# Kernel tuning notes

Measured on AMD Instinct MI355X. Metric: run time of the kernel, lower is better.

## Reference

```python
import jax, jax.numpy as jnp
import numpy as np

NUM_PHONEMES = 512
D = 128  # embed_dim == hidden_channels == out_channels (forced by residuals)
N = 50000
E = 500000
PAD_ID = 0
LN_EPS = 1e-5


def setup_inputs() -> dict:
    key = jax.random.key(0)
    ks = jax.random.split(key, 12)
    node_ids = jax.random.randint(ks[0], (N,), 0, NUM_PHONEMES)
    edge_index = jax.random.randint(ks[1], (2, E), 0, N)
    emb = jax.random.normal(ks[2], (NUM_PHONEMES, D), jnp.float32) * 0.05
    emb = emb.at[PAD_ID].set(0.0)  # padding_idx row zeroed
    W1 = jax.random.normal(ks[3], (D, D), jnp.float32) * (1.0 / np.sqrt(D))
    b1 = jnp.zeros((D,), jnp.float32)
    W2 = jax.random.normal(ks[4], (D, D), jnp.float32) * (1.0 / np.sqrt(D))
    b2 = jnp.zeros((D,), jnp.float32)
    g1 = jnp.ones((D,), jnp.float32)
    beta1 = jnp.zeros((D,), jnp.float32)
    g2 = jnp.ones((D,), jnp.float32)
    beta2 = jnp.zeros((D,), jnp.float32)
    return {"node_ids": node_ids, "edge_index": edge_index, "emb": emb,
            "W1": W1, "b1": b1, "W2": W2, "b2": b2,
            "g1": g1, "beta1": beta1, "g2": g2, "beta2": beta2}


def _gcn_conv(x, src, dst, W, b):
    """PyG GCNConv with add_self_loops=True, normalize=True.
    out = D^{-1/2} (A + I) D^{-1/2} (x W) + b, deg computed after self-loops."""
    n = x.shape[0]
    loop = jnp.arange(n, dtype=src.dtype)
    src_f = jnp.concatenate([src, loop])  # [E+N]
    dst_f = jnp.concatenate([dst, loop])
    deg = jax.ops.segment_sum(jnp.ones_like(dst_f, dtype=x.dtype), dst_f,
                              num_segments=n)  # >=1 due to self-loops
    dis = jax.lax.rsqrt(deg)
    norm = dis[src_f] * dis[dst_f]  # [E+N]
    h = x @ W  # [N, D_out]
    msg = h[src_f] * norm[:, None]  # [E+N, D_out] gather (memory-bound)
    out = jax.ops.segment_sum(msg, dst_f, num_segments=n)  # scatter-add
    return out + b


def _layernorm(x, g, b):
    mu = jnp.mean(x, axis=-1, keepdims=True)
    var = jnp.mean(jnp.square(x - mu), axis=-1, keepdims=True)
    return (x - mu) * jax.lax.rsqrt(var + LN_EPS) * g + b


def reference(node_ids, edge_index, emb, W1, b1, W2, b2, g1, beta1, g2, beta2):
    src, dst = edge_index[0], edge_index[1]
    x = emb[node_ids]  # embedding lookup [N, D]
    h1 = _gcn_conv(x, src, dst, W1, b1)
    x = _layernorm(x + h1, g1, beta1)  # dropout is identity in eval mode
    h2 = _gcn_conv(x, src, dst, W2, b2)
    x = _layernorm(x + h2, g2, beta2)
    return x
```

## Files before the change

### kernel.cpp

```cpp
#include <hip/hip_runtime.h>

#define DD 128
#define CAP 32
#define SPILL_MAX 4096

typedef __attribute__((ext_vector_type(8))) short short8;
typedef __attribute__((ext_vector_type(4))) float float4v;

static __device__ __forceinline__ unsigned short f2bf(float x) {
    unsigned u = __builtin_bit_cast(unsigned, x);
    u += 0x7fffu + ((u >> 16) & 1u);
    return (unsigned short)(u >> 16);
}
static __device__ __forceinline__ float bflo(unsigned u) {
    return __builtin_bit_cast(float, u << 16);
}
static __device__ __forceinline__ float bfhi(unsigned u) {
    return __builtin_bit_cast(float, u & 0xffff0000u);
}

__global__ __launch_bounds__(256) void k_init(const float* __restrict__ emb,
                                              const float* __restrict__ W1,
                                              const float* __restrict__ W2,
                                              unsigned* __restrict__ embW1b,
                                              unsigned short* __restrict__ Wb,
                                              const int* __restrict__ src,
                                              const int* __restrict__ dst,
                                              const int* __restrict__ node_ids,
                                              int* __restrict__ cursor,
                                              unsigned* __restrict__ recs,
                                              int* __restrict__ spillCnt,
                                              int* __restrict__ spill_d,
                                              int* __restrict__ spill_r, int E) {
    int blk = blockIdx.x;
    if (blk < 128) {
        int w = threadIdx.x >> 6;
        int t = threadIdx.x & 63;
        int p = blk * 4 + w;
        int c0 = t * 2, c1 = t * 2 + 1;
        float s0 = 0.f, s1 = 0.f;
#pragma unroll 8
        for (int k = 0; k < DD; k++) {
            float e = emb[p * DD + k];
            s0 += e * W1[k * DD + c0];
            s1 += e * W1[k * DD + c1];
        }
        embW1b[p * 64 + t] = (unsigned)f2bf(s0) | ((unsigned)f2bf(s1) << 16);
    } else if (blk < 136) {
        int t = (blk - 128) * 256 + threadIdx.x;
        int nt = t >> 8, ks = (t >> 6) & 3, lane = t & 63;
        int n = nt * 16 + (lane & 15);
        int kbase = ks * 32 + (lane >> 4) * 8;
        unsigned short* o = Wb + (size_t)t * 8;
#pragma unroll
        for (int j = 0; j < 8; j++)
            o[j] = f2bf(W2[(kbase + j) * DD + n]);
    } else {
        int base = ((blk - 136) * 256 + threadIdx.x) * 4;
        if (base >= E) return;
#pragma unroll
        for (int u = 0; u < 4; u++) {
            int e = base + u;
            if (e >= E) break;
            int s = src[e], d = dst[e];
            unsigned rec = (unsigned)s | ((unsigned)node_ids[s] << 16);
            int pos = atomicAdd(&cursor[d], 1);
            if (pos < CAP) {
                recs[(size_t)d * CAP + pos] = rec;
            } else {
                int sp = atomicAdd(spillCnt, 1);
                if (sp < SPILL_MAX) { spill_d[sp] = d; spill_r[sp] = (int)rec; }
            }
        }
    }
}

__global__ __launch_bounds__(256, 4) void k_node1(const int* __restrict__ cursor,
                                               const unsigned* __restrict__ recs,
                                               const int* __restrict__ node_ids,
                                               const float* __restrict__ emb,
                                               const unsigned* __restrict__ embW1b,
                                               const int* __restrict__ spillCnt,
                                               const int* __restrict__ spill_d,
                                               const int* __restrict__ spill_r,
                                               const float* __restrict__ b1,
                                               const float* __restrict__ g1,
                                               const float* __restrict__ beta1,
                                               unsigned* __restrict__ x1b,
                                               float* __restrict__ disf, int N) {
    int gid = blockIdx.x * blockDim.x + threadIdx.x;
    int wave = gid >> 6;
    int lane = threadIdx.x & 63;
    int qtr = lane >> 4;
    int l = lane & 15;
    int qbase = lane & 48;
    int i = wave * 4 + qtr;
    if (i >= N) return;
    int dg = cursor[i];
    int dgc = (dg < CAP) ? dg : CAP;
    unsigned rv0 = recs[(size_t)i * CAP + l];
    unsigned rv1 = recs[(size_t)i * CAP + 16 + l];
    int c = l * 8;
    float a0 = 0.f, a1 = 0.f, a2 = 0.f, a3 = 0.f, a4 = 0.f, a5 = 0.f, a6 = 0.f, a7 = 0.f;
    for (int j0 = 0; j0 < dgc; j0 += 8) {
        unsigned rvs = (j0 < 16) ? rv0 : rv1;
        const uint4* ap[8]; const int* cp[8]; float nn[8];
#pragma unroll
        for (int q = 0; q < 8; q++) {
            int e = j0 + q;
            int ec = (e < dgc) ? e : (dgc - 1);
            unsigned rec = __shfl(rvs, qbase + (ec & 15), 64);
            nn[q] = (e < dgc) ? 1.f : 0.f;
            ap[q] = (const uint4*)(embW1b + ((rec >> 16) & 511u) * 64 + l * 4);
            cp[q] = cursor + (rec & 0xFFFFu);
        }
        uint4 buf[8]; int cb[8];
#pragma unroll
        for (int q = 0; q < 8; q++) { buf[q] = *ap[q]; cb[q] = *cp[q]; }
#pragma unroll
        for (int q = 0; q < 8; q++) {
            float n = rsqrtf((float)cb[q] + 1.f) * nn[q];
            uint4 a = buf[q];
            a0 += bflo(a.x) * n; a1 += bfhi(a.x) * n;
            a2 += bflo(a.y) * n; a3 += bfhi(a.y) * n;
            a4 += bflo(a.z) * n; a5 += bfhi(a.z) * n;
            a6 += bflo(a.w) * n; a7 += bfhi(a.w) * n;
        }
    }
    if (dg > CAP) {
        int sc = *spillCnt; if (sc > SPILL_MAX) sc = SPILL_MAX;
        for (int j = 0; j < sc; j++) {
            if (spill_d[j] == i) {
                unsigned rec = (unsigned)spill_r[j];
                int s = rec & 0xFFFFu;
                float n = rsqrtf((float)cursor[s] + 1.0f);
                uint4 a = *(const uint4*)(embW1b + ((rec >> 16) & 511u) * 64 + l * 4);
                a0 += bflo(a.x) * n; a1 += bfhi(a.x) * n;
                a2 += bflo(a.y) * n; a3 += bfhi(a.y) * n;
                a4 += bflo(a.z) * n; a5 += bfhi(a.z) * n;
                a6 += bflo(a.w) * n; a7 += bfhi(a.w) * n;
            }
        }
    }
    float di = rsqrtf((float)dg + 1.0f);
    int pid = node_ids[i];
    float4 ev0 = *(const float4*)(emb + (size_t)pid * DD + c);
    float4 ev1 = *(const float4*)(emb + (size_t)pid * DD + c + 4);
    uint4 hw = *(const uint4*)(embW1b + pid * 64 + l * 4);
    float4 bb0 = *(const float4*)(b1 + c);
    float4 bb1 = *(const float4*)(b1 + c + 4);
    float v0 = ev0.x + di * (a0 + di * bflo(hw.x)) + bb0.x;
    float v1 = ev0.y + di * (a1 + di * bfhi(hw.x)) + bb0.y;
    float v2 = ev0.z + di * (a2 + di * bflo(hw.y)) + bb0.z;
    float v3 = ev0.w + di * (a3 + di * bfhi(hw.y)) + bb0.w;
    float v4 = ev1.x + di * (a4 + di * bflo(hw.z)) + bb1.x;
    float v5 = ev1.y + di * (a5 + di * bfhi(hw.z)) + bb1.y;
    float v6 = ev1.z + di * (a6 + di * bflo(hw.w)) + bb1.z;
    float v7 = ev1.w + di * (a7 + di * bfhi(hw.w)) + bb1.w;
    float sum = v0 + v1 + v2 + v3 + v4 + v5 + v6 + v7;
#pragma unroll
    for (int o = 8; o >= 1; o >>= 1) sum += __shfl_xor(sum, o, 64);
    float mu = sum * (1.f / DD);
    float d0 = v0 - mu, d1 = v1 - mu, d2 = v2 - mu, d3 = v3 - mu;
    float d4 = v4 - mu, d5 = v5 - mu, d6 = v6 - mu, d7 = v7 - mu;
    float ss = d0 * d0 + d1 * d1 + d2 * d2 + d3 * d3 + d4 * d4 + d5 * d5 + d6 * d6 + d7 * d7;
#pragma unroll
    for (int o = 8; o >= 1; o >>= 1) ss += __shfl_xor(ss, o, 64);
    float r = rsqrtf(ss * (1.f / DD) + 1e-5f);
    float4 gg0 = *(const float4*)(g1 + c);
    float4 gg1 = *(const float4*)(g1 + c + 4);
    float4 be0 = *(const float4*)(beta1 + c);
    float4 be1 = *(const float4*)(beta1 + c + 4);
    float o0 = d0 * r * gg0.x + be0.x;
    float o1 = d1 * r * gg0.y + be0.y;
    float o2 = d2 * r * gg0.z + be0.z;
    float o3 = d3 * r * gg0.w + be0.w;
    float o4 = d4 * r * gg1.x + be1.x;
    float o5 = d5 * r * gg1.y + be1.y;
    float o6 = d6 * r * gg1.z + be1.z;
    float o7 = d7 * r * gg1.w + be1.w;
    uint4 pk;
    pk.x = (unsigned)f2bf(o0) | ((unsigned)f2bf(o1) << 16);
    pk.y = (unsigned)f2bf(o2) | ((unsigned)f2bf(o3) << 16);
    pk.z = (unsigned)f2bf(o4) | ((unsigned)f2bf(o5) << 16);
    pk.w = (unsigned)f2bf(o6) | ((unsigned)f2bf(o7) << 16);
    *(uint4*)(x1b + (size_t)i * 64 + l * 4) = pk;
    if (l == 0) disf[i] = di;
}

__global__ __launch_bounds__(256, 4) void k_node2(const int* __restrict__ cursor,
                                               const unsigned* __restrict__ recs,
                                               const unsigned* __restrict__ x1b,
                                               const float* __restrict__ disf,
                                               const int* __restrict__ spillCnt,
                                               const int* __restrict__ spill_d,
                                               const int* __restrict__ spill_r,
                                               const float* __restrict__ b2,
                                               const float* __restrict__ g2,
                                               const float* __restrict__ beta2,
                                               const unsigned short* __restrict__ Wb,
                                               float* __restrict__ out, int N) {
    __shared__ unsigned tileA[4][16 * 68];
    int wv = threadIdx.x >> 6;
    int lane = threadIdx.x & 63;
    int qtr = lane >> 4;
    int l = lane & 15;
    int qbase = lane & 48;
    int wbase = (blockIdx.x * 4 + wv) * 16;
    unsigned* myT = &tileA[wv][0];
#pragma unroll 1
    for (int k = 0; k < 4; k++) {
        int rr = k * 4 + qtr;
        int i = wbase + rr;
        uint4 pk = make_uint4(0, 0, 0, 0);
        if (i < N) {
            int dg = cursor[i];
            int dgc = (dg < CAP) ? dg : CAP;
            unsigned rv0 = recs[(size_t)i * CAP + l];
            unsigned rv1 = recs[(size_t)i * CAP + 16 + l];
            float a0 = 0.f, a1 = 0.f, a2 = 0.f, a3 = 0.f, a4 = 0.f, a5 = 0.f, a6 = 0.f, a7 = 0.f;
            for (int j0 = 0; j0 < dgc; j0 += 8) {
                unsigned rvs = (j0 < 16) ? rv0 : rv1;
                const uint4* ap[8]; const float* fp[8]; float nn[8];
#pragma unroll
                for (int q = 0; q < 8; q++) {
                    int e = j0 + q;
                    int ec = (e < dgc) ? e : (dgc - 1);
                    unsigned rec = __shfl(rvs, qbase + (ec & 15), 64);
                    unsigned s = rec & 0xFFFFu;
                    nn[q] = (e < dgc) ? 1.f : 0.f;
                    ap[q] = (const uint4*)(x1b + (size_t)s * 64 + l * 4);
                    fp[q] = disf + s;
                }
                uint4 buf[8]; float fb[8];
#pragma unroll
                for (int q = 0; q < 8; q++) { buf[q] = *ap[q]; fb[q] = *fp[q]; }
#pragma unroll
                for (int q = 0; q < 8; q++) {
                    float n = fb[q] * nn[q];
                    uint4 a = buf[q];
                    a0 += bflo(a.x) * n; a1 += bfhi(a.x) * n;
                    a2 += bflo(a.y) * n; a3 += bfhi(a.y) * n;
                    a4 += bflo(a.z) * n; a5 += bfhi(a.z) * n;
                    a6 += bflo(a.w) * n; a7 += bfhi(a.w) * n;
                }
            }
            if (dg > CAP) {
                int sc = *spillCnt; if (sc > SPILL_MAX) sc = SPILL_MAX;
                for (int j = 0; j < sc; j++) {
                    if (spill_d[j] == i) {
                        unsigned s = (unsigned)spill_r[j] & 0xFFFFu;
                        float n = disf[s];
                        uint4 a = *(const uint4*)(x1b + (size_t)s * 64 + l * 4);
                        a0 += bflo(a.x) * n; a1 += bfhi(a.x) * n;
                        a2 += bflo(a.y) * n; a3 += bfhi(a.y) * n;
                        a4 += bflo(a.z) * n; a5 += bfhi(a.z) * n;
                        a6 += bflo(a.w) * n; a7 += bfhi(a.w) * n;
                    }
                }
            }
            float di = disf[i];
            uint4 xv = *(const uint4*)(x1b + (size_t)i * 64 + l * 4);
            float z0 = a0 + di * bflo(xv.x);
            float z1 = a1 + di * bfhi(xv.x);
            float z2 = a2 + di * bflo(xv.y);
            float z3 = a3 + di * bfhi(xv.y);
            float z4 = a4 + di * bflo(xv.z);
            float z5 = a5 + di * bfhi(xv.z);
            float z6 = a6 + di * bflo(xv.w);
            float z7 = a7 + di * bfhi(xv.w);
            pk.x = (unsigned)f2bf(z0) | ((unsigned)f2bf(z1) << 16);
            pk.y = (unsigned)f2bf(z2) | ((unsigned)f2bf(z3) << 16);
            pk.z = (unsigned)f2bf(z4) | ((unsigned)f2bf(z5) << 16);
            pk.w = (unsigned)f2bf(z6) | ((unsigned)f2bf(z7) << 16);
        }
        *(uint4*)(myT + rr * 68 + l * 4) = pk;
    }
    __syncthreads();
    short8 afr[4];
    const char* tb = (const char*)myT;
#pragma unroll
    for (int ks = 0; ks < 4; ks++)
        afr[ks] = *(const short8*)(tb + l * 272 + ks * 64 + qtr * 16);
    const short8* bp = (const short8*)Wb;
    float4v acc[8];
#pragma unroll
    for (int nt = 0; nt < 8; nt++) {
        float4v a = {0.f, 0.f, 0.f, 0.f};
#pragma unroll
        for (int ks = 0; ks < 4; ks++)
            a = __builtin_amdgcn_mfma_f32_16x16x32_bf16(afr[ks], bp[(nt * 4 + ks) * 64 + lane], a, 0, 0, 0);
        acc[nt] = a;
    }
    float dvarr[4];
    {
        float4 dv4 = *(const float4*)(disf + wbase + qtr * 4);
        dvarr[0] = dv4.x; dvarr[1] = dv4.y; dvarr[2] = dv4.z; dvarr[3] = dv4.w;
    }
#pragma unroll
    for (int r = 0; r < 4; r++) {
        int rowg = wbase + qtr * 4 + r;
        if (rowg < N) {
            float di = dvarr[r];
            float vv[8]; float sum = 0.f;
#pragma unroll
            for (int nt = 0; nt < 8; nt++) {
                unsigned xw = x1b[(size_t)rowg * 64 + nt * 8 + (l >> 1)];
                float xr = (l & 1) ? bfhi(xw) : bflo(xw);
                vv[nt] = xr + di * acc[nt][r] + b2[nt * 16 + l];
                sum += vv[nt];
            }
#pragma unroll
            for (int o = 8; o >= 1; o >>= 1) sum += __shfl_xor(sum, o, 64);
            float mu = sum * (1.f / DD);
            float ss = 0.f;
#pragma unroll
            for (int nt = 0; nt < 8; nt++) { float d = vv[nt] - mu; vv[nt] = d; ss += d * d; }
#pragma unroll
            for (int o = 8; o >= 1; o >>= 1) ss += __shfl_xor(ss, o, 64);
            float rstd = rsqrtf(ss * (1.f / DD) + 1e-5f);
#pragma unroll
            for (int nt = 0; nt < 8; nt++)
                out[(size_t)rowg * DD + nt * 16 + l] = vv[nt] * rstd * g2[nt * 16 + l] + beta2[nt * 16 + l];
        }
    }
}

extern "C" void kernel_launch(void* const* d_in, const int* in_sizes, int n_in,
                              void* d_out, int out_size, void* d_ws, size_t ws_size,
                              hipStream_t stream) {
    const int* node_ids = (const int*)d_in[0];
    const int* edge_index = (const int*)d_in[1];
    const float* emb   = (const float*)d_in[2];
    const float* W1    = (const float*)d_in[3];
    const float* b1    = (const float*)d_in[4];
    const float* W2    = (const float*)d_in[5];
    const float* b2    = (const float*)d_in[6];
    const float* g1    = (const float*)d_in[7];
    const float* beta1 = (const float*)d_in[8];
    const float* g2    = (const float*)d_in[9];
    const float* beta2 = (const float*)d_in[10];
    const int N = in_sizes[0];
    const int E = in_sizes[1] / 2;
    const int* srcp = edge_index;
    const int* dstp = edge_index + E;
    float* out = (float*)d_out;

    char* base = (char*)d_ws;
    size_t off = 0;
    auto carve = [&](size_t bytes) -> void* {
        void* p = base + off;
        off += (bytes + 255) & ~(size_t)255;
        return p;
    };
    int*      meta   = (int*)carve((size_t)(N + 17) * 4);
    int*      cursor = meta;
    int*      spillCnt = meta + N + 16;
    int*      spill_d = (int*)carve((size_t)SPILL_MAX * 4);
    int*      spill_r = (int*)carve((size_t)SPILL_MAX * 4);
    unsigned* recs   = (unsigned*)carve((size_t)N * CAP * 4);
    unsigned* embW1b = (unsigned*)carve((size_t)512 * 64 * 4);
    unsigned* x1b    = (unsigned*)carve((size_t)(N + 64) * 64 * 4);
    float*    disf   = (float*)carve((size_t)(N + 64) * 4);
    unsigned short* Wb = (unsigned short*)carve((size_t)DD * DD * 2);
    (void)ws_size; (void)n_in; (void)out_size;

    const int TB = 256;
    const int Hb = (E + 1023) / 1024;

    hipMemsetAsync(meta, 0, (size_t)(N + 17) * 4, stream);
    k_init<<<136 + Hb, TB, 0, stream>>>(emb, W1, W2, embW1b, Wb,
                                        srcp, dstp, node_ids, cursor, recs,
                                        spillCnt, spill_d, spill_r, E);

    long long tn = (long long)((N + 3) / 4) * 64;
    int nodeBlocks = (int)((tn + TB - 1) / TB);
    k_node1<<<nodeBlocks, TB, 0, stream>>>(cursor, recs, node_ids, emb, embW1b,
                                           spillCnt, spill_d, spill_r,
                                           b1, g1, beta1, x1b, disf, N);
    int blocks64 = (N + 63) / 64;
    k_node2<<<blocks64, TB, 0, stream>>>(cursor, recs, x1b, disf,
                                         spillCnt, spill_d, spill_r,
                                         b2, g2, beta2, Wb, out, N);
}
```

Baseline: 167.3 us.

## Restructure k_node2 to 16 rows per block with split-N MFMA and LDS epilogue

k_node2 now handles 16 rows per 256-thread block instead of 64, with each wave aggregating one neighbour row per quarter-wave in a single pass rather than looping over four rows. The 16x128 MFMA output is split across the four waves (two column tiles each) and staged through a shared fp32 tile, so the LayerNorm epilogue reads contiguous 8-column chunks and writes vectorised float4 outputs. The aim is more blocks and more gather parallelism for latency hiding, plus coalesced output stores. The cost is an extra block barrier and LDS round trip, and four times as many blocks launched.

```diff
diff --git a/kernel.cpp b/kernel.cpp
--- a/kernel.cpp
+++ b/kernel.cpp
@@ -200,130 +200,148 @@
                                                const float* __restrict__ beta2,
                                                const unsigned short* __restrict__ Wb,
                                                float* __restrict__ out, int N) {
-    __shared__ unsigned tileA[4][16 * 68];
+    __shared__ unsigned tileA[16 * 68];
+    __shared__ float tileH[16 * 132];
     int wv = threadIdx.x >> 6;
     int lane = threadIdx.x & 63;
     int qtr = lane >> 4;
     int l = lane & 15;
     int qbase = lane & 48;
-    int wbase = (blockIdx.x * 4 + wv) * 16;
-    unsigned* myT = &tileA[wv][0];
-#pragma unroll 1
-    for (int k = 0; k < 4; k++) {
-        int rr = k * 4 + qtr;
-        int i = wbase + rr;
-        uint4 pk = make_uint4(0, 0, 0, 0);
-        if (i < N) {
-            int dg = cursor[i];
-            int dgc = (dg < CAP) ? dg : CAP;
-            unsigned rv0 = recs[(size_t)i * CAP + l];
-            unsigned rv1 = recs[(size_t)i * CAP + 16 + l];
-            float a0 = 0.f, a1 = 0.f, a2 = 0.f, a3 = 0.f, a4 = 0.f, a5 = 0.f, a6 = 0.f, a7 = 0.f;
-            for (int j0 = 0; j0 < dgc; j0 += 8) {
-                unsigned rvs = (j0 < 16) ? rv0 : rv1;
-                const uint4* ap[8]; const float* fp[8]; float nn[8];
-#pragma unroll
-                for (int q = 0; q < 8; q++) {
-                    int e = j0 + q;
-                    int ec = (e < dgc) ? e : (dgc - 1);
-                    unsigned rec = __shfl(rvs, qbase + (ec & 15), 64);
-                    unsigned s = rec & 0xFFFFu;
-                    nn[q] = (e < dgc) ? 1.f : 0.f;
-                    ap[q] = (const uint4*)(x1b + (size_t)s * 64 + l * 4);
-                    fp[q] = disf + s;
-                }
-                uint4 buf[8]; float fb[8];
-#pragma unroll
-                for (int q = 0; q < 8; q++) { buf[q] = *ap[q]; fb[q] = *fp[q]; }
-#pragma unroll
-                for (int q = 0; q < 8; q++) {
-                    float n = fb[q] * nn[q];
-                    uint4 a = buf[q];
+    int base16 = blockIdx.x * 16;
+    int rr = wv * 4 + qtr;
+    int i = base16 + rr;
+    int c = l * 8;
+    uint4 xv = make_uint4(0, 0, 0, 0);
+    float di = 0.f;
+    uint4 pk = make_uint4(0, 0, 0, 0);
+    if (i < N) {
+        int dg = cursor[i];
+        int dgc = (dg < CAP) ? dg : CAP;
+        unsigned rv0 = recs[(size_t)i * CAP + l];
+        unsigned rv1 = recs[(size_t)i * CAP + 16 + l];
+        float a0 = 0.f, a1 = 0.f, a2 = 0.f, a3 = 0.f, a4 = 0.f, a5 = 0.f, a6 = 0.f, a7 = 0.f;
+        for (int j0 = 0; j0 < dgc; j0 += 8) {
+            unsigned rvs = (j0 < 16) ? rv0 : rv1;
+            const uint4* ap[8]; const float* fp[8]; float nn[8];
+#pragma unroll
+            for (int q = 0; q < 8; q++) {
+                int e = j0 + q;
+                int ec = (e < dgc) ? e : (dgc - 1);
+                unsigned rec = __shfl(rvs, qbase + (ec & 15), 64);
+                unsigned s = rec & 0xFFFFu;
+                nn[q] = (e < dgc) ? 1.f : 0.f;
+                ap[q] = (const uint4*)(x1b + (size_t)s * 64 + l * 4);
+                fp[q] = disf + s;
+            }
+            uint4 buf[8]; float fb[8];
+#pragma unroll
+            for (int q = 0; q < 8; q++) { buf[q] = *ap[q]; fb[q] = *fp[q]; }
+#pragma unroll
+            for (int q = 0; q < 8; q++) {
+                float n = fb[q] * nn[q];
+                uint4 a = buf[q];
+                a0 += bflo(a.x) * n; a1 += bfhi(a.x) * n;
+                a2 += bflo(a.y) * n; a3 += bfhi(a.y) * n;
+                a4 += bflo(a.z) * n; a5 += bfhi(a.z) * n;
+                a6 += bflo(a.w) * n; a7 += bfhi(a.w) * n;
+            }
+        }
+        if (dg > CAP) {
+            int sc = *spillCnt; if (sc > SPILL_MAX) sc = SPILL_MAX;
+            for (int j = 0; j < sc; j++) {
+                if (spill_d[j] == i) {
+                    unsigned s = (unsigned)spill_r[j] & 0xFFFFu;
+                    float n = disf[s];
+                    uint4 a = *(const uint4*)(x1b + (size_t)s * 64 + l * 4);
                     a0 += bflo(a.x) * n; a1 += bfhi(a.x) * n;
                     a2 += bflo(a.y) * n; a3 += bfhi(a.y) * n;
                     a4 += bflo(a.z) * n; a5 += bfhi(a.z) * n;
                     a6 += bflo(a.w) * n; a7 += bfhi(a.w) * n;
                 }
             }
-            if (dg > CAP) {
-                int sc = *spillCnt; if (sc > SPILL_MAX) sc = SPILL_MAX;
-                for (int j = 0; j < sc; j++) {
-                    if (spill_d[j] == i) {
-                        unsigned s = (unsigned)spill_r[j] & 0xFFFFu;
-                        float n = disf[s];
-                        uint4 a = *(const uint4*)(x1b + (size_t)s * 64 + l * 4);
-                        a0 += bflo(a.x) * n; a1 += bfhi(a.x) * n;
-                        a2 += bflo(a.y) * n; a3 += bfhi(a.y) * n;
-                        a4 += bflo(a.z) * n; a5 += bfhi(a.z) * n;
-                        a6 += bflo(a.w) * n; a7 += bfhi(a.w) * n;
-                    }
-                }
-            }
-            float di = disf[i];
-            uint4 xv = *(const uint4*)(x1b + (size_t)i * 64 + l * 4);
-            float z0 = a0 + di * bflo(xv.x);
-            float z1 = a1 + di * bfhi(xv.x);
-            float z2 = a2 + di * bflo(xv.y);
-            float z3 = a3 + di * bfhi(xv.y);
-            float z4 = a4 + di * bflo(xv.z);
-            float z5 = a5 + di * bfhi(xv.z);
-            float z6 = a6 + di * bflo(xv.w);
-            float z7 = a7 + di * bfhi(xv.w);
-            pk.x = (unsigned)f2bf(z0) | ((unsigned)f2bf(z1) << 16);
-            pk.y = (unsigned)f2bf(z2) | ((unsigned)f2bf(z3) << 16);
-            pk.z = (unsigned)f2bf(z4) | ((unsigned)f2bf(z5) << 16);
-            pk.w = (unsigned)f2bf(z6) | ((unsigned)f2bf(z7) << 16);
-        }
-        *(uint4*)(myT + rr * 68 + l * 4) = pk;
+        }
+        di = disf[i];
+        xv = *(const uint4*)(x1b + (size_t)i * 64 + l * 4);
+        float z0 = a0 + di * bflo(xv.x);
+        float z1 = a1 + di * bfhi(xv.x);
+        float z2 = a2 + di * bflo(xv.y);
+        float z3 = a3 + di * bfhi(xv.y);
+        float z4 = a4 + di * bflo(xv.z);
+        float z5 = a5 + di * bfhi(xv.z);
+        float z6 = a6 + di * bflo(xv.w);
+        float z7 = a7 + di * bfhi(xv.w);
+        pk.x = (unsigned)f2bf(z0) | ((unsigned)f2bf(z1) << 16);
+        pk.y = (unsigned)f2bf(z2) | ((unsigned)f2bf(z3) << 16);
+        pk.z = (unsigned)f2bf(z4) | ((unsigned)f2bf(z5) << 16);
+        pk.w = (unsigned)f2bf(z6) | ((unsigned)f2bf(z7) << 16);
+    }
+    *(uint4*)(tileA + rr * 68 + l * 4) = pk;
+    __syncthreads();
+    {
+        short8 afr[4];
+        const char* tb = (const char*)tileA;
+#pragma unroll
+        for (int ks = 0; ks < 4; ks++)
+            afr[ks] = *(const short8*)(tb + l * 272 + ks * 64 + qtr * 16);
+        float dr[4];
+#pragma unroll
+        for (int r = 0; r < 4; r++) {
+            int rw = base16 + qtr * 4 + r;
+            dr[r] = (rw < N) ? disf[rw] : 0.f;
+        }
+        const short8* bp = (const short8*)Wb;
+#pragma unroll
+        for (int t = 0; t < 2; t++) {
+            int nt = wv * 2 + t;
+            float4v acc = {0.f, 0.f, 0.f, 0.f};
+#pragma unroll
+            for (int ks = 0; ks < 4; ks++)
+                acc = __builtin_amdgcn_mfma_f32_16x16x32_bf16(afr[ks], bp[(nt * 4 + ks) * 64 + lane], acc, 0, 0, 0);
+            int col = nt * 16 + l;
+#pragma unroll
+            for (int r = 0; r < 4; r++)
+                tileH[(qtr * 4 + r) * 132 + col] = acc[r] * dr[r];
+        }
     }
     __syncthreads();
-    short8 afr[4];
-    const char* tb = (const char*)myT;
-#pragma unroll
-    for (int ks = 0; ks < 4; ks++)
-        afr[ks] = *(const short8*)(tb + l * 272 + ks * 64 + qtr * 16);
-    const short8* bp = (const short8*)Wb;
-    float4v acc[8];
-#pragma unroll
-    for (int nt = 0; nt < 8; nt++) {
-        float4v a = {0.f, 0.f, 0.f, 0.f};
-#pragma unroll
-        for (int ks = 0; ks < 4; ks++)
-            a = __builtin_amdgcn_mfma_f32_16x16x32_bf16(afr[ks], bp[(nt * 4 + ks) * 64 + lane], a, 0, 0, 0);
-        acc[nt] = a;
-    }
-    float dvarr[4];
-    {
-        float4 dv4 = *(const float4*)(disf + wbase + qtr * 4);
-        dvarr[0] = dv4.x; dvarr[1] = dv4.y; dvarr[2] = dv4.z; dvarr[3] = dv4.w;
-    }
-#pragma unroll
-    for (int r = 0; r < 4; r++) {
-        int rowg = wbase + qtr * 4 + r;
-        if (rowg < N) {
-            float di = dvarr[r];
-            float vv[8]; float sum = 0.f;
-#pragma unroll
-            for (int nt = 0; nt < 8; nt++) {
-                unsigned xw = x1b[(size_t)rowg * 64 + nt * 8 + (l >> 1)];
-                float xr = (l & 1) ? bfhi(xw) : bflo(xw);
-                vv[nt] = xr + di * acc[nt][r] + b2[nt * 16 + l];
-                sum += vv[nt];
-            }
-#pragma unroll
-            for (int o = 8; o >= 1; o >>= 1) sum += __shfl_xor(sum, o, 64);
-            float mu = sum * (1.f / DD);
-            float ss = 0.f;
-#pragma unroll
-            for (int nt = 0; nt < 8; nt++) { float d = vv[nt] - mu; vv[nt] = d; ss += d * d; }
-#pragma unroll
-            for (int o = 8; o >= 1; o >>= 1) ss += __shfl_xor(ss, o, 64);
-            float rstd = rsqrtf(ss * (1.f / DD) + 1e-5f);
-#pragma unroll
-            for (int nt = 0; nt < 8; nt++)
-                out[(size_t)rowg * DD + nt * 16 + l] = vv[nt] * rstd * g2[nt * 16 + l] + beta2[nt * 16 + l];
-        }
-    }
+    if (i >= N) return;
+    float4 h0 = *(const float4*)(tileH + rr * 132 + c);
+    float4 h1 = *(const float4*)(tileH + rr * 132 + c + 4);
+    float4 bb0 = *(const float4*)(b2 + c);
+    float4 bb1 = *(const float4*)(b2 + c + 4);
+    float v0 = bflo(xv.x) + h0.x + bb0.x;
+    float v1 = bfhi(xv.x) + h0.y + bb0.y;
+    float v2 = bflo(xv.y) + h0.z + bb0.z;
+    float v3 = bfhi(xv.y) + h0.w + bb0.w;
+    float v4 = bflo(xv.z) + h1.x + bb1.x;
+    float v5 = bfhi(xv.z) + h1.y + bb1.y;
+    float v6 = bflo(xv.w) + h1.z + bb1.z;
+    float v7 = bfhi(xv.w) + h1.w + bb1.w;
+    float sum = v0 + v1 + v2 + v3 + v4 + v5 + v6 + v7;
+#pragma unroll
+    for (int o = 8; o >= 1; o >>= 1) sum += __shfl_xor(sum, o, 64);
+    float mu = sum * (1.f / DD);
+    float d0 = v0 - mu, d1 = v1 - mu, d2 = v2 - mu, d3 = v3 - mu;
+    float d4 = v4 - mu, d5 = v5 - mu, d6 = v6 - mu, d7 = v7 - mu;
+    float ss = d0 * d0 + d1 * d1 + d2 * d2 + d3 * d3 + d4 * d4 + d5 * d5 + d6 * d6 + d7 * d7;
+#pragma unroll
+    for (int o = 8; o >= 1; o >>= 1) ss += __shfl_xor(ss, o, 64);
+    float rstd = rsqrtf(ss * (1.f / DD) + 1e-5f);
+    float4 gg0 = *(const float4*)(g2 + c);
+    float4 gg1 = *(const float4*)(g2 + c + 4);
+    float4 be0 = *(const float4*)(beta2 + c);
+    float4 be1 = *(const float4*)(beta2 + c + 4);
+    float4 o0, o1;
+    o0.x = d0 * rstd * gg0.x + be0.x;
+    o0.y = d1 * rstd * gg0.y + be0.y;
+    o0.z = d2 * rstd * gg0.z + be0.z;
+    o0.w = d3 * rstd * gg0.w + be0.w;
+    o1.x = d4 * rstd * gg1.x + be1.x;
+    o1.y = d5 * rstd * gg1.y + be1.y;
+    o1.z = d6 * rstd * gg1.z + be1.z;
+    o1.w = d7 * rstd * gg1.w + be1.w;
+    *(float4*)(out + (size_t)i * DD + c) = o0;
+    *(float4*)(out + (size_t)i * DD + c + 4) = o1;
 }
 
 extern "C" void kernel_launch(void* const* d_in, const int* in_sizes, int n_in,
@@ -378,8 +396,8 @@
     k_node1<<<nodeBlocks, TB, 0, stream>>>(cursor, recs, node_ids, emb, embW1b,
                                            spillCnt, spill_d, spill_r,
                                            b1, g1, beta1, x1b, disf, N);
-    int blocks64 = (N + 63) / 64;
-    k_node2<<<blocks64, TB, 0, stream>>>(cursor, recs, x1b, disf,
+    int blocks16 = (N + 15) / 16;
+    k_node2<<<blocks16, TB, 0, stream>>>(cursor, recs, x1b, disf,
                                          spillCnt, spill_d, spill_r,
                                          b2, g2, beta2, Wb, out, N);
 }
```

New measurement: 160.8 us. 1.04x faster.
